# Kernel tuning notes

Measured on AMD Instinct MI355X. Metric: run time of the kernel, lower is better.

## Reference

```python
import jax, jax.numpy as jnp
import numpy as np

N = 100000   # nodes
E = 1600000  # edges (avg degree 16)
D = 128      # feature dim (layer_sizes = [128, 128, 128])


def setup_inputs() -> dict:
    key = jax.random.key(0)
    ks = jax.random.split(key, 8)
    s = 1.0 / np.sqrt(D)  # glorot-ish scale for linear weights
    return {
        "x": jax.random.normal(ks[0], (N, D), jnp.float32),
        "edge_index": jax.random.randint(ks[1], (2, E), 0, N, dtype=jnp.int32),
        "perturb_first": jax.random.normal(ks[2], (N, D), jnp.float32) * 0.01,
        "perturb_last": jax.random.normal(ks[3], (N, D), jnp.float32) * 0.01,
        "W1": jax.random.normal(ks[4], (D, D), jnp.float32) * s,
        "b1": jnp.zeros((D,), jnp.float32),
        "W2": jax.random.normal(ks[5], (D, D), jnp.float32) * s,
        "b2": jnp.zeros((D,), jnp.float32),
    }


def reference(x, edge_index, perturb_first, perturb_last, W1, b1, W2, b2):
    n = x.shape[0]
    # PyG GCNConv: add self-loops, symmetric deg^{-1/2} normalization.
    loop = jnp.arange(n, dtype=edge_index.dtype)
    src = jnp.concatenate([edge_index[0], loop])  # [E+N]
    dst = jnp.concatenate([edge_index[1], loop])  # [E+N]
    deg = jax.ops.segment_sum(jnp.ones(dst.shape[0], x.dtype), dst, num_segments=n)
    dinv = jnp.where(deg > 0, 1.0 / jnp.sqrt(deg), 0.0)
    norm = (dinv[src] * dinv[dst])[:, None]  # [E+N, 1]

    def gcn_conv(h, W, b):
        h = h @ W.T                                   # linear (bias-free), [N, D]
        msg = h[src] * norm                           # gather + scale, [E+N, D]
        out = jax.ops.segment_sum(msg, dst, num_segments=n)  # scatter-add
        return out + b

    # forward only runs model[0] and model[3] (the two GCNConv layers);
    # norms and PReLU are skipped by the original forward.
    h = gcn_conv(x, W1, b1) + perturb_first
    out = gcn_conv(h, W2, b2) + perturb_last
    return out
```

## Files before the change

kernel.cpp:

```cpp
#include <hip/hip_runtime.h>
#include <math.h>

#define D 128
#define WS_PAD 132

typedef short bf16x8 __attribute__((ext_vector_type(8)));
typedef float f32x4 __attribute__((ext_vector_type(4)));

__device__ __forceinline__ unsigned short f2bf(float f) {
  unsigned u = __float_as_uint(f);
  u += 0x7FFFu + ((u >> 16) & 1u);
  return (unsigned short)(u >> 16);
}

__device__ __forceinline__ float bf2f(unsigned short h) {
  return __uint_as_float(((unsigned)h) << 16);
}

__device__ __forceinline__ float bflo(unsigned u) { return __uint_as_float(u << 16); }
__device__ __forceinline__ float bfhi(unsigned u) { return __uint_as_float(u & 0xFFFF0000u); }


__global__ __launch_bounds__(256) void count_deg_kernel(const int* __restrict__ dst, int E,
                                                        int* __restrict__ deg,
                                                        int* __restrict__ rank,
                                                        const float* __restrict__ W2,
                                                        unsigned short* __restrict__ W2bf,
                                                        const float* __restrict__ W1,
                                                        unsigned short* __restrict__ W1h,
                                                        unsigned short* __restrict__ W1l) {
  int nbe = (E + 1023) >> 10;
  int b = blockIdx.x;
  if (b >= nbe) {
    if (W2bf == nullptr) return;
    int which = b - nbe;
    if (which < 8) {
      int t = which * 256 + threadIdx.x;
      #pragma unroll
      for (int q = 0; q < 2; ++q) {
        int idx = t + q * 2048;
        float4 w = ((const float4*)W2)[idx];
        ushort4 o;
        o.x = f2bf(w.x); o.y = f2bf(w.y); o.z = f2bf(w.z); o.w = f2bf(w.w);
        ((ushort4*)W2bf)[idx] = o;
      }
    } else {
      int t = (which - 8) * 256 + threadIdx.x;
      #pragma unroll
      for (int q = 0; q < 2; ++q) {
        int idx = t + q * 2048;
        float4 w = ((const float4*)W1)[idx];
        ushort4 hi, lo;
        hi.x = f2bf(w.x); lo.x = f2bf(w.x - bf2f(hi.x));
        hi.y = f2bf(w.y); lo.y = f2bf(w.y - bf2f(hi.y));
        hi.z = f2bf(w.z); lo.z = f2bf(w.z - bf2f(hi.z));
        hi.w = f2bf(w.w); lo.w = f2bf(w.w - bf2f(hi.w));
        ((ushort4*)W1h)[idx] = hi;
        ((ushort4*)W1l)[idx] = lo;
      }
    }
    return;
  }
  int e0 = (b * 256 + threadIdx.x) * 4;
  if (rank != nullptr) {
    if (e0 + 4 <= E && ((E & 3) == 0)) {
      int4 d = *(const int4*)(dst + e0);
      int r0 = atomicAdd(&deg[d.x], 1);
      int r1 = atomicAdd(&deg[d.y], 1);
      int r2 = atomicAdd(&deg[d.z], 1);
      int r3 = atomicAdd(&deg[d.w], 1);
      *(int4*)(rank + e0) = make_int4(r0, r1, r2, r3);
    } else {
      for (int e = e0; e < E && e < e0 + 4; ++e) rank[e] = atomicAdd(&deg[dst[e]], 1);
    }
  } else {
    for (int e = e0; e < E && e < e0 + 4; ++e) atomicAdd(&deg[dst[e]], 1);
  }
}


__global__ __launch_bounds__(256) void scan_blocksum_kernel(const int* __restrict__ deg, int n,
                                                            int* __restrict__ blockSums) {
  __shared__ int sm[256];
  int t = threadIdx.x;
  int i = blockIdx.x * 256 + t;
  sm[t] = (i < n) ? deg[i] : 0;
  __syncthreads();
  for (int off = 128; off > 0; off >>= 1) {
    if (t < off) sm[t] += sm[t + off];
    __syncthreads();
  }
  if (t == 0) blockSums[blockIdx.x] = sm[0];
}

__global__ __launch_bounds__(512) void scan_top_kernel(int* __restrict__ blockSums, int nb) {
  __shared__ int sm[512];
  int t = threadIdx.x;
  int v = (t < nb) ? blockSums[t] : 0;
  sm[t] = v;
  __syncthreads();
  for (int off = 1; off < 512; off <<= 1) {
    int x = (t >= off) ? sm[t - off] : 0;
    __syncthreads();
    sm[t] += x;
    __syncthreads();
  }
  if (t < nb) blockSums[t] = sm[t] - v;
}

__global__ __launch_bounds__(256) void scan_write_kernel(const int* __restrict__ deg, int n,
                                                         const int* __restrict__ blockSums,
                                                         int* __restrict__ ptr,
                                                         float* __restrict__ dinv) {
  __shared__ int sm[256];
  int t = threadIdx.x;
  int i = blockIdx.x * 256 + t;
  int v = (i < n) ? deg[i] : 0;
  sm[t] = v;
  __syncthreads();
  for (int off = 1; off < 256; off <<= 1) {
    int x = (t >= off) ? sm[t - off] : 0;
    __syncthreads();
    sm[t] += x;
    __syncthreads();
  }
  if (i < n) {
    int ex = blockSums[blockIdx.x] + sm[t] - v;
    ptr[i] = ex;
    dinv[i] = 1.0f / sqrtf((float)(v + 1));
    if (i == n - 1) ptr[n] = ex + v;
  }
}


__device__ __forceinline__ void gemm_body(const float* __restrict__ X,
                                          const float* __restrict__ W,
                                          const float* __restrict__ dinv,
                                          unsigned short* __restrict__ H, int n,
                                          int bid, int nblocks,
                                          float* __restrict__ Ws, float* __restrict__ Xs) {
  const int tid = threadIdx.x;
  const int tx = tid & 31;
  const int ty = tid >> 5;
  const int ntiles = (n + 31) >> 5;

  for (int tile = bid; tile < ntiles; tile += nblocks) {
    const int row0 = tile << 5;
    const int rows_here = min(32, n - row0);
    __syncthreads();
    {
      const float4* Xg = (const float4*)(X + (size_t)row0 * D);
      int tmax = rows_here * 32;
      for (int t = tid; t < tmax; t += 256) ((float4*)Xs)[t] = Xg[t];
    }
    float acc[4][4] = {{0.f}};
    #pragma unroll
    for (int kt = 0; kt < 128; kt += 64) {
      __syncthreads();
      for (int t = tid; t < 2048; t += 256) {
        int j  = t >> 4;
        int k4 = (t & 15) << 2;
        float4 w = ((const float4*)W)[j * 32 + (kt >> 2) + (t & 15)];
        Ws[(k4 + 0) * WS_PAD + j] = w.x;
        Ws[(k4 + 1) * WS_PAD + j] = w.y;
        Ws[(k4 + 2) * WS_PAD + j] = w.z;
        Ws[(k4 + 3) * WS_PAD + j] = w.w;
      }
      __syncthreads();
      #pragma unroll 4
      for (int k = 0; k < 64; ++k) {
        float4 w = *(const float4*)&Ws[k * WS_PAD + (tx << 2)];
        #pragma unroll
        for (int r = 0; r < 4; ++r) {
          float xv = Xs[(ty + 8 * r) * 128 + (kt + k)];
          acc[r][0] += xv * w.x;
          acc[r][1] += xv * w.y;
          acc[r][2] += xv * w.z;
          acc[r][3] += xv * w.w;
        }
      }
    }
    #pragma unroll
    for (int r = 0; r < 4; ++r) {
      int row = row0 + ty + 8 * r;
      if (row < n) {
        float s = dinv[row];
        unsigned h0 = f2bf(s * acc[r][0]);
        unsigned h1 = f2bf(s * acc[r][1]);
        unsigned h2 = f2bf(s * acc[r][2]);
        unsigned h3 = f2bf(s * acc[r][3]);
        ((uint2*)(H + (size_t)row * D))[tx] = make_uint2(h0 | (h1 << 16), h2 | (h3 << 16));
      }
    }
  }
}


__global__ __launch_bounds__(256) void fused_fill_gemm_kernel(
    const int* __restrict__ src, const int* __restrict__ dst,
    int* __restrict__ ptr, int* __restrict__ csr, int E,
    const float* __restrict__ X, const float* __restrict__ W,
    const float* __restrict__ dinv, unsigned short* __restrict__ H, int n) {
  __shared__ float Ws[64 * WS_PAD];
  __shared__ float Xs[32 * 128];
  int sub = blockIdx.x & 7;
  if (sub < 2) {
    int fb = (blockIdx.x >> 3) * 2 + sub;
    int stride = 512 * 256;
    for (int e = fb * 256 + threadIdx.x; e < E; e += stride) {
      int d = dst[e];
      int pos = atomicAdd(&ptr[d], 1);
      csr[pos] = src[e];
    }
  } else {
    int gb = (blockIdx.x >> 3) * 6 + (sub - 2);
    gemm_body(X, W, dinv, H, n, gb, 1536, Ws, Xs);
  }
}

__global__ __launch_bounds__(256) void gemm128_kernel(const float* __restrict__ X,
                                                      const float* __restrict__ W,
                                                      const float* __restrict__ dinv,
                                                      unsigned short* __restrict__ H, int n) {
  __shared__ float Ws[64 * WS_PAD];
  __shared__ float Xs[32 * 128];
  gemm_body(X, W, dinv, H, n, blockIdx.x, gridDim.x, Ws, Xs);
}


#define FUSED_GRID 2048
#define G1_PITCH 136

__global__ __launch_bounds__(256) void fused_fill_mfma_kernel(
    const int* __restrict__ src, const int* __restrict__ dst,
    const int* __restrict__ ptr, const int* __restrict__ rank,
    int* __restrict__ csr, int E,
    const float* __restrict__ X,
    const unsigned short* __restrict__ W1h, const unsigned short* __restrict__ W1l,
    const float* __restrict__ dinv, unsigned short* __restrict__ H, int n) {
  __shared__ unsigned short Ths[32 * G1_PITCH];
  __shared__ unsigned short Tls[32 * G1_PITCH];
  int sub = blockIdx.x & 7;
  if (sub < 2) {
    int fb = (blockIdx.x >> 3) * 2 + sub;
    const int T8 = 512 * 256 * 8;
    int t = fb * 256 + threadIdx.x;
    const bool al16 = ((E & 3) == 0);
    for (int e0 = t * 8; e0 < E; e0 += T8) {
      if (e0 + 8 <= E && al16) {
        int4 d0 = ((const int4*)(dst + e0))[0];
        int4 d1 = ((const int4*)(dst + e0))[1];
        int4 s0 = ((const int4*)(src + e0))[0];
        int4 s1 = ((const int4*)(src + e0))[1];
        int4 r0 = ((const int4*)(rank + e0))[0];
        int4 r1 = ((const int4*)(rank + e0))[1];
        int p0 = ptr[d0.x] + r0.x;
        int p1 = ptr[d0.y] + r0.y;
        int p2 = ptr[d0.z] + r0.z;
        int p3 = ptr[d0.w] + r0.w;
        int p4 = ptr[d1.x] + r1.x;
        int p5 = ptr[d1.y] + r1.y;
        int p6 = ptr[d1.z] + r1.z;
        int p7 = ptr[d1.w] + r1.w;
        csr[p0] = s0.x; csr[p1] = s0.y; csr[p2] = s0.z; csr[p3] = s0.w;
        csr[p4] = s1.x; csr[p5] = s1.y; csr[p6] = s1.z; csr[p7] = s1.w;
      } else {
        for (int e = e0; e < E && e < e0 + 8; ++e)
          csr[ptr[dst[e]] + rank[e]] = src[e];
      }
    }
  } else {
    int gb = (blockIdx.x >> 3) * 6 + (sub - 2);
    const int tid = threadIdx.x;
    const int wv = tid >> 6;
    const int lane = tid & 63;
    const int m = lane & 15;
    const int quad = lane >> 4;
    const int mt = wv >> 1;
    const int ntb = (wv & 1) * 4;
    const int ntiles = (n + 31) >> 5;

    for (int tile = gb; tile < ntiles; tile += 1536) {
      const int row0 = tile << 5;
      const int rows_here = min(32, n - row0);
      __syncthreads();
      {
        const float4* Xg = (const float4*)(X + (size_t)row0 * D);
        int tmax = rows_here * 32;
        for (int t = tid; t < tmax; t += 256) {
          float4 xv = Xg[t];
          int r = t >> 5, c4 = (t & 31) << 2;
          ushort4 hi, lo;
          hi.x = f2bf(xv.x); lo.x = f2bf(xv.x - bf2f(hi.x));
          hi.y = f2bf(xv.y); lo.y = f2bf(xv.y - bf2f(hi.y));
          hi.z = f2bf(xv.z); lo.z = f2bf(xv.z - bf2f(hi.z));
          hi.w = f2bf(xv.w); lo.w = f2bf(xv.w - bf2f(hi.w));
          *(ushort4*)&Ths[r * G1_PITCH + c4] = hi;
          *(ushort4*)&Tls[r * G1_PITCH + c4] = lo;
        }
      }
      __syncthreads();

      f32x4 acc0 = {0.f, 0.f, 0.f, 0.f};
      f32x4 acc1 = {0.f, 0.f, 0.f, 0.f};
      f32x4 acc2 = {0.f, 0.f, 0.f, 0.f};
      f32x4 acc3 = {0.f, 0.f, 0.f, 0.f};
      #pragma unroll
      for (int s = 0; s < 4; ++s) {
        int k = (s << 5) + (quad << 3);
        bf16x8 ah = *(const bf16x8*)&Ths[(mt * 16 + m) * G1_PITCH + k];
        bf16x8 al = *(const bf16x8*)&Tls[(mt * 16 + m) * G1_PITCH + k];
        bf16x8 bh0 = *(const bf16x8*)&W1h[(size_t)((ntb + 0) * 16 + m) * 128 + k];
        bf16x8 bl0 = *(const bf16x8*)&W1l[(size_t)((ntb + 0) * 16 + m) * 128 + k];
        acc0 = __builtin_amdgcn_mfma_f32_16x16x32_bf16(ah, bh0, acc0, 0, 0, 0);
        acc0 = __builtin_amdgcn_mfma_f32_16x16x32_bf16(al, bh0, acc0, 0, 0, 0);
        acc0 = __builtin_amdgcn_mfma_f32_16x16x32_bf16(ah, bl0, acc0, 0, 0, 0);
        bf16x8 bh1 = *(const bf16x8*)&W1h[(size_t)((ntb + 1) * 16 + m) * 128 + k];
        bf16x8 bl1 = *(const bf16x8*)&W1l[(size_t)((ntb + 1) * 16 + m) * 128 + k];
        acc1 = __builtin_amdgcn_mfma_f32_16x16x32_bf16(ah, bh1, acc1, 0, 0, 0);
        acc1 = __builtin_amdgcn_mfma_f32_16x16x32_bf16(al, bh1, acc1, 0, 0, 0);
        acc1 = __builtin_amdgcn_mfma_f32_16x16x32_bf16(ah, bl1, acc1, 0, 0, 0);
        bf16x8 bh2 = *(const bf16x8*)&W1h[(size_t)((ntb + 2) * 16 + m) * 128 + k];
        bf16x8 bl2 = *(const bf16x8*)&W1l[(size_t)((ntb + 2) * 16 + m) * 128 + k];
        acc2 = __builtin_amdgcn_mfma_f32_16x16x32_bf16(ah, bh2, acc2, 0, 0, 0);
        acc2 = __builtin_amdgcn_mfma_f32_16x16x32_bf16(al, bh2, acc2, 0, 0, 0);
        acc2 = __builtin_amdgcn_mfma_f32_16x16x32_bf16(ah, bl2, acc2, 0, 0, 0);
        bf16x8 bh3 = *(const bf16x8*)&W1h[(size_t)((ntb + 3) * 16 + m) * 128 + k];
        bf16x8 bl3 = *(const bf16x8*)&W1l[(size_t)((ntb + 3) * 16 + m) * 128 + k];
        acc3 = __builtin_amdgcn_mfma_f32_16x16x32_bf16(ah, bh3, acc3, 0, 0, 0);
        acc3 = __builtin_amdgcn_mfma_f32_16x16x32_bf16(al, bh3, acc3, 0, 0, 0);
        acc3 = __builtin_amdgcn_mfma_f32_16x16x32_bf16(ah, bl3, acc3, 0, 0, 0);
      }
      #pragma unroll
      for (int r = 0; r < 4; ++r) {
        int row = mt * 16 + (quad << 2) + r;
        int g = row0 + row;
        if (g < n) {
          float sc = dinv[g];
          H[(size_t)g * D + (ntb + 0) * 16 + m] = f2bf(sc * acc0[r]);
          H[(size_t)g * D + (ntb + 1) * 16 + m] = f2bf(sc * acc1[r]);
          H[(size_t)g * D + (ntb + 2) * 16 + m] = f2bf(sc * acc2[r]);
          H[(size_t)g * D + (ntb + 3) * 16 + m] = f2bf(sc * acc3[r]);
        }
      }
    }
  }
}


__device__ __forceinline__ void gather_quad(const int* __restrict__ csr, int start, int end,
                                            const uint4* __restrict__ Hu4, int i, int sub,
                                            float acc[8]) {
  uint4 v = Hu4[(size_t)i * 16 + sub];
  acc[0] = bflo(v.x); acc[1] = bfhi(v.x);
  acc[2] = bflo(v.y); acc[3] = bfhi(v.y);
  acc[4] = bflo(v.z); acc[5] = bfhi(v.z);
  acc[6] = bflo(v.w); acc[7] = bfhi(v.w);
  int e = start;
  while (__ballot(e < end)) {
    uint4 w0 = {0u, 0u, 0u, 0u}, w1 = {0u, 0u, 0u, 0u};
    if (e < end)     w0 = Hu4[(size_t)csr[e] * 16 + sub];
    if (e + 1 < end) w1 = Hu4[(size_t)csr[e + 1] * 16 + sub];
    acc[0] += bflo(w0.x); acc[1] += bfhi(w0.x);
    acc[2] += bflo(w0.y); acc[3] += bfhi(w0.y);
    acc[4] += bflo(w0.z); acc[5] += bfhi(w0.z);
    acc[6] += bflo(w0.w); acc[7] += bfhi(w0.w);
    acc[0] += bflo(w1.x); acc[1] += bfhi(w1.x);
    acc[2] += bflo(w1.y); acc[3] += bfhi(w1.y);
    acc[4] += bflo(w1.z); acc[5] += bfhi(w1.z);
    acc[6] += bflo(w1.w); acc[7] += bfhi(w1.w);
    e += 2;
  }
}


__device__ __forceinline__ void gather_row_legacy(const int* __restrict__ csr, int start, int end,
                                                  const unsigned* __restrict__ Hu,
                                                  int i, int lane, float& ax, float& ay) {
  unsigned v = Hu[(size_t)i * 64 + lane];
  ax = __uint_as_float(v << 16);
  ay = __uint_as_float(v & 0xFFFF0000u);
  for (int e = start; e < end; ++e) {
    unsigned w = Hu[(size_t)csr[e] * 64 + lane];
    ax += __uint_as_float(w << 16);
    ay += __uint_as_float(w & 0xFFFF0000u);
  }
}


__global__ __launch_bounds__(256, 8) void gather_kernel(const int* __restrict__ csr,
                                                        const int* __restrict__ rptr,
                                                        const float* __restrict__ dinv,
                                                        const unsigned* __restrict__ Hu,
                                                        const float* __restrict__ bias,
                                                        const float* __restrict__ perturb,
                                                        float* __restrict__ out, int n) {
  const int lane = threadIdx.x & 63;
  const int g = lane >> 4;
  const int sub = lane & 15;
  int i = (blockIdx.x << 4) + ((threadIdx.x >> 6) << 2) + g;
  bool valid = i < n;
  int ic = valid ? i : (n - 1);
  int start = rptr[ic];
  int end = valid ? rptr[ic + 1] : start;
  float acc[8];
  gather_quad(csr, start, end, (const uint4*)Hu, ic, sub, acc);
  if (valid) {
    float di = dinv[i];
    float4 b0 = *(const float4*)&bias[sub * 8];
    float4 b1 = *(const float4*)&bias[sub * 8 + 4];
    float4 p0 = *(const float4*)&perturb[(size_t)i * D + sub * 8];
    float4 p1 = *(const float4*)&perturb[(size_t)i * D + sub * 8 + 4];
    float4 o0, o1;
    o0.x = b0.x + p0.x + di * acc[0];
    o0.y = b0.y + p0.y + di * acc[1];
    o0.z = b0.z + p0.z + di * acc[2];
    o0.w = b0.w + p0.w + di * acc[3];
    o1.x = b1.x + p1.x + di * acc[4];
    o1.y = b1.y + p1.y + di * acc[5];
    o1.z = b1.z + p1.z + di * acc[6];
    o1.w = b1.w + p1.w + di * acc[7];
    *(float4*)&out[(size_t)i * D + sub * 8] = o0;
    *(float4*)&out[(size_t)i * D + sub * 8 + 4] = o1;
  }
}

__global__ __launch_bounds__(256, 8) void gather_kernel_old(const int* __restrict__ csr,
                                                            const int* __restrict__ rend,
                                                            const float* __restrict__ dinv,
                                                            const unsigned* __restrict__ Hu,
                                                            const float* __restrict__ bias,
                                                            const float* __restrict__ perturb,
                                                            float* __restrict__ out, int n) {
  int i = (blockIdx.x << 2) + (threadIdx.x >> 6);
  if (i >= n) return;
  int lane = threadIdx.x & 63;
  int start = (i == 0) ? 0 : rend[i - 1];
  float ax, ay;
  gather_row_legacy(csr, start, rend[i], Hu, i, lane, ax, ay);
  float di = dinv[i];
  float2 p = ((const float2*)(perturb + (size_t)i * D))[lane];
  float2 o;
  o.x = bias[2 * lane + 0] + p.x + di * ax;
  o.y = bias[2 * lane + 1] + p.y + di * ay;
  ((float2*)(out + (size_t)i * D))[lane] = o;
}


#define GG_PITCH 136

__global__ __launch_bounds__(512, 8) void gather_gemm_kernel(
    const int* __restrict__ csr, const int* __restrict__ rptr,
    const float* __restrict__ dinv, const unsigned* __restrict__ Hu,
    const float* __restrict__ bias, const float* __restrict__ perturb,
    const unsigned short* __restrict__ W2bf, unsigned short* __restrict__ H2, int n) {
  __shared__ unsigned short Ts[32 * GG_PITCH];
  const int tid = threadIdx.x;
  const int wv = tid >> 6;
  const int lane = tid & 63;
  const int base = blockIdx.x << 5;

  {
    const int g = lane >> 4;
    const int sub = lane & 15;
    int row_in_block = (wv << 2) + g;
    int i = base + row_in_block;
    bool valid = i < n;
    int ic = valid ? i : (n - 1);
    int start = rptr[ic];
    int end = valid ? rptr[ic + 1] : start;
    float acc[8];
    gather_quad(csr, start, end, (const uint4*)Hu, ic, sub, acc);
    if (valid) {
      float di = dinv[i];
      float4 b0 = *(const float4*)&bias[sub * 8];
      float4 b1 = *(const float4*)&bias[sub * 8 + 4];
      float4 p0 = *(const float4*)&perturb[(size_t)i * D + sub * 8];
      float4 p1 = *(const float4*)&perturb[(size_t)i * D + sub * 8 + 4];
      unsigned q0 = (unsigned)f2bf(b0.x + p0.x + di * acc[0]) |
                    ((unsigned)f2bf(b0.y + p0.y + di * acc[1]) << 16);
      unsigned q1 = (unsigned)f2bf(b0.z + p0.z + di * acc[2]) |
                    ((unsigned)f2bf(b0.w + p0.w + di * acc[3]) << 16);
      unsigned q2 = (unsigned)f2bf(b1.x + p1.x + di * acc[4]) |
                    ((unsigned)f2bf(b1.y + p1.y + di * acc[5]) << 16);
      unsigned q3 = (unsigned)f2bf(b1.z + p1.z + di * acc[6]) |
                    ((unsigned)f2bf(b1.w + p1.w + di * acc[7]) << 16);
      uint4 pack = make_uint4(q0, q1, q2, q3);
      *(uint4*)&Ts[row_in_block * GG_PITCH + sub * 8] = pack;
    }
  }
  __syncthreads();

  const int mt = wv >> 2;
  const int nt0 = wv & 3;
  const int m = lane & 15;
  const int quad = lane >> 4;
  const unsigned short* Wrow0 = W2bf + (size_t)(nt0 * 16 + m) * 128;
  const unsigned short* Wrow1 = W2bf + (size_t)((nt0 + 4) * 16 + m) * 128;
  f32x4 acc0 = {0.f, 0.f, 0.f, 0.f};
  f32x4 acc1 = {0.f, 0.f, 0.f, 0.f};
  #pragma unroll
  for (int s = 0; s < 4; ++s) {
    int k = (s << 5) + (quad << 3);
    bf16x8 a  = *(const bf16x8*)&Ts[(mt * 16 + m) * GG_PITCH + k];
    bf16x8 b0 = *(const bf16x8*)&Wrow0[k];
    bf16x8 b1 = *(const bf16x8*)&Wrow1[k];
    acc0 = __builtin_amdgcn_mfma_f32_16x16x32_bf16(a, b0, acc0, 0, 0, 0);
    acc1 = __builtin_amdgcn_mfma_f32_16x16x32_bf16(a, b1, acc1, 0, 0, 0);
  }
  #pragma unroll
  for (int r = 0; r < 4; ++r) {
    int row = mt * 16 + (quad << 2) + r;
    int gg = base + row;
    if (gg < n) {
      float s = dinv[gg];
      H2[(size_t)gg * D + nt0 * 16 + m]       = f2bf(s * acc0[r]);
      H2[(size_t)gg * D + (nt0 + 4) * 16 + m] = f2bf(s * acc1[r]);
    }
  }
}


extern "C" void kernel_launch(void* const* d_in, const int* in_sizes, int n_in,
                              void* d_out, int out_size, void* d_ws, size_t ws_size,
                              hipStream_t stream) {
  const float* x  = (const float*)d_in[0];
  const int*   ei = (const int*)d_in[1];
  const float* pf = (const float*)d_in[2];
  const float* pl = (const float*)d_in[3];
  const float* W1 = (const float*)d_in[4];
  const float* b1 = (const float*)d_in[5];
  const float* W2 = (const float*)d_in[6];
  const float* b2 = (const float*)d_in[7];
  float* out = (float*)d_out;

  const int n = in_sizes[0] / D;
  const int E = in_sizes[1] / 2;
  const int* src = ei;
  const int* dst = ei + E;

  int*   deg       = (int*)d_ws;
  float* dinv      = (float*)d_ws + n;
  int*   ptr       = (int*)d_ws + 2 * n;
  int*   blockSums = (int*)d_ws + 3 * n + 1;
  int*   csr       = (int*)d_ws + 3 * n + 1 + 512;
  size_t a1_off = ((size_t)(3 * n + 1 + 512 + E) * 4 + 255) & ~(size_t)255;
  unsigned short* A1 = (unsigned short*)((char*)d_ws + a1_off);
  unsigned short* A2 = A1 + (size_t)n * D;
  unsigned short* W2bf = A2 + (size_t)n * D;
  unsigned short* W1h  = W2bf + 128 * 128;
  unsigned short* W1l  = W1h + 128 * 128;
  int* rank = (int*)A2;
  size_t needed = a1_off + (2 * (size_t)n * D + 3 * 128 * 128) * sizeof(unsigned short);
  const bool fused_l2 = (ws_size >= needed);

  const int nb_n = (n + 255) / 256;
  const int nb_e4 = (E + 1023) / 1024;
  const int nb_g16 = (n + 15) / 16;
  const int nb_g4 = (n + 3) / 4;

  hipMemsetAsync(deg, 0, (size_t)n * sizeof(int), stream);
  count_deg_kernel<<<nb_e4 + 16, 256, 0, stream>>>(
      dst, E, deg, fused_l2 ? rank : (int*)nullptr, W2,
      fused_l2 ? W2bf : (unsigned short*)nullptr, W1, W1h, W1l);
  scan_blocksum_kernel<<<nb_n, 256, 0, stream>>>(deg, n, blockSums);
  scan_top_kernel<<<1, 512, 0, stream>>>(blockSums, nb_n);
  scan_write_kernel<<<nb_n, 256, 0, stream>>>(deg, n, blockSums, ptr, dinv);

  if (fused_l2) {
    fused_fill_mfma_kernel<<<FUSED_GRID, 256, 0, stream>>>(src, dst, ptr, rank, csr, E, x,
                                                           W1h, W1l, dinv, A1, n);
    gather_gemm_kernel<<<(n + 31) / 32, 512, 0, stream>>>(csr, ptr, dinv, (const unsigned*)A1,
                                                          b1, pf, W2bf, A2, n);
    gather_kernel<<<nb_g16, 256, 0, stream>>>(csr, ptr, dinv, (const unsigned*)A2, b2, pl, out, n);
  } else {
    fused_fill_gemm_kernel<<<FUSED_GRID, 256, 0, stream>>>(src, dst, ptr, csr, E, x, W1, dinv, A1, n);
    gather_kernel_old<<<nb_g4, 256, 0, stream>>>(csr, ptr, dinv, (const unsigned*)A1, b1, pf, out, n);
    gemm128_kernel<<<1024, 256, 0, stream>>>(out, W2, dinv, A1, n);
    gather_kernel_old<<<nb_g4, 256, 0, stream>>>(csr, ptr, dinv, (const unsigned*)A1, b2, pl, out, n);
  }
}
```

Measured before the change: 490.5 us.

## Overlap degree counting with layer-1 GEMM and apply source normalization in gather

The layer-1 MFMA GEMM now writes unscaled X·W1 and runs fused with the degree-count atomics, so it no longer waits for the degree scan and dinv. The per-source dinv scaling moves into the first gather, which now loads dinv[j] for every neighbor, and CSR fill becomes its own kernel after the scan. Weight conversion is split out into a small separate kernel. The trade is an extra random dinv load per edge in gather 1 and one more launch, in exchange for overlapping the atomic-heavy count with the GEMM.

New measurement: 460.2 us. -6.2%, faster.

```diff
diff --git a/kernel.cpp b/kernel.cpp
--- a/kernel.cpp
+++ b/kernel.cpp
@@ -21,256 +21,70 @@
 __device__ __forceinline__ float bfhi(unsigned u) { return __uint_as_float(u & 0xFFFF0000u); }
 
 
-__global__ __launch_bounds__(256) void count_deg_kernel(const int* __restrict__ dst, int E,
-                                                        int* __restrict__ deg,
-                                                        int* __restrict__ rank,
-                                                        const float* __restrict__ W2,
-                                                        unsigned short* __restrict__ W2bf,
-                                                        const float* __restrict__ W1,
-                                                        unsigned short* __restrict__ W1h,
-                                                        unsigned short* __restrict__ W1l) {
-  int nbe = (E + 1023) >> 10;
-  int b = blockIdx.x;
-  if (b >= nbe) {
-    if (W2bf == nullptr) return;
-    int which = b - nbe;
-    if (which < 8) {
-      int t = which * 256 + threadIdx.x;
-      #pragma unroll
-      for (int q = 0; q < 2; ++q) {
-        int idx = t + q * 2048;
-        float4 w = ((const float4*)W2)[idx];
-        ushort4 o;
-        o.x = f2bf(w.x); o.y = f2bf(w.y); o.z = f2bf(w.z); o.w = f2bf(w.w);
-        ((ushort4*)W2bf)[idx] = o;
-      }
-    } else {
-      int t = (which - 8) * 256 + threadIdx.x;
-      #pragma unroll
-      for (int q = 0; q < 2; ++q) {
-        int idx = t + q * 2048;
-        float4 w = ((const float4*)W1)[idx];
-        ushort4 hi, lo;
-        hi.x = f2bf(w.x); lo.x = f2bf(w.x - bf2f(hi.x));
-        hi.y = f2bf(w.y); lo.y = f2bf(w.y - bf2f(hi.y));
-        hi.z = f2bf(w.z); lo.z = f2bf(w.z - bf2f(hi.z));
-        hi.w = f2bf(w.w); lo.w = f2bf(w.w - bf2f(hi.w));
-        ((ushort4*)W1h)[idx] = hi;
-        ((ushort4*)W1l)[idx] = lo;
-      }
-    }
-    return;
-  }
-  int e0 = (b * 256 + threadIdx.x) * 4;
-  if (rank != nullptr) {
-    if (e0 + 4 <= E && ((E & 3) == 0)) {
-      int4 d = *(const int4*)(dst + e0);
-      int r0 = atomicAdd(&deg[d.x], 1);
-      int r1 = atomicAdd(&deg[d.y], 1);
-      int r2 = atomicAdd(&deg[d.z], 1);
-      int r3 = atomicAdd(&deg[d.w], 1);
-      *(int4*)(rank + e0) = make_int4(r0, r1, r2, r3);
-    } else {
-      for (int e = e0; e < E && e < e0 + 4; ++e) rank[e] = atomicAdd(&deg[dst[e]], 1);
+__global__ __launch_bounds__(256) void wprep_kernel(const float* __restrict__ W2,
+                                                    unsigned short* __restrict__ W2bf,
+                                                    const float* __restrict__ W1,
+                                                    unsigned short* __restrict__ W1h,
+                                                    unsigned short* __restrict__ W1l) {
+  int which = blockIdx.x;
+  if (which < 8) {
+    int t = which * 256 + threadIdx.x;
+    #pragma unroll
+    for (int q = 0; q < 2; ++q) {
+      int idx = t + q * 2048;
+      float4 w = ((const float4*)W2)[idx];
+      ushort4 o;
+      o.x = f2bf(w.x); o.y = f2bf(w.y); o.z = f2bf(w.z); o.w = f2bf(w.w);
+      ((ushort4*)W2bf)[idx] = o;
     }
   } else {
-    for (int e = e0; e < E && e < e0 + 4; ++e) atomicAdd(&deg[dst[e]], 1);
-  }
-}
-
-
-__global__ __launch_bounds__(256) void scan_blocksum_kernel(const int* __restrict__ deg, int n,
-                                                            int* __restrict__ blockSums) {
-  __shared__ int sm[256];
-  int t = threadIdx.x;
-  int i = blockIdx.x * 256 + t;
-  sm[t] = (i < n) ? deg[i] : 0;
-  __syncthreads();
-  for (int off = 128; off > 0; off >>= 1) {
-    if (t < off) sm[t] += sm[t + off];
-    __syncthreads();
-  }
-  if (t == 0) blockSums[blockIdx.x] = sm[0];
-}
-
-__global__ __launch_bounds__(512) void scan_top_kernel(int* __restrict__ blockSums, int nb) {
-  __shared__ int sm[512];
-  int t = threadIdx.x;
-  int v = (t < nb) ? blockSums[t] : 0;
-  sm[t] = v;
-  __syncthreads();
-  for (int off = 1; off < 512; off <<= 1) {
-    int x = (t >= off) ? sm[t - off] : 0;
-    __syncthreads();
-    sm[t] += x;
-    __syncthreads();
-  }
-  if (t < nb) blockSums[t] = sm[t] - v;
-}
-
-__global__ __launch_bounds__(256) void scan_write_kernel(const int* __restrict__ deg, int n,
-                                                         const int* __restrict__ blockSums,
-                                                         int* __restrict__ ptr,
-                                                         float* __restrict__ dinv) {
-  __shared__ int sm[256];
-  int t = threadIdx.x;
-  int i = blockIdx.x * 256 + t;
-  int v = (i < n) ? deg[i] : 0;
-  sm[t] = v;
-  __syncthreads();
-  for (int off = 1; off < 256; off <<= 1) {
-    int x = (t >= off) ? sm[t - off] : 0;
-    __syncthreads();
-    sm[t] += x;
-    __syncthreads();
-  }
-  if (i < n) {
-    int ex = blockSums[blockIdx.x] + sm[t] - v;
-    ptr[i] = ex;
-    dinv[i] = 1.0f / sqrtf((float)(v + 1));
-    if (i == n - 1) ptr[n] = ex + v;
-  }
-}
-
-
-__device__ __forceinline__ void gemm_body(const float* __restrict__ X,
-                                          const float* __restrict__ W,
-                                          const float* __restrict__ dinv,
-                                          unsigned short* __restrict__ H, int n,
-                                          int bid, int nblocks,
-                                          float* __restrict__ Ws, float* __restrict__ Xs) {
-  const int tid = threadIdx.x;
-  const int tx = tid & 31;
-  const int ty = tid >> 5;
-  const int ntiles = (n + 31) >> 5;
-
-  for (int tile = bid; tile < ntiles; tile += nblocks) {
-    const int row0 = tile << 5;
-    const int rows_here = min(32, n - row0);
-    __syncthreads();
-    {
-      const float4* Xg = (const float4*)(X + (size_t)row0 * D);
-      int tmax = rows_here * 32;
-      for (int t = tid; t < tmax; t += 256) ((float4*)Xs)[t] = Xg[t];
-    }
-    float acc[4][4] = {{0.f}};
+    int t = (which - 8) * 256 + threadIdx.x;
     #pragma unroll
-    for (int kt = 0; kt < 128; kt += 64) {
-      __syncthreads();
-      for (int t = tid; t < 2048; t += 256) {
-        int j  = t >> 4;
-        int k4 = (t & 15) << 2;
-        float4 w = ((const float4*)W)[j * 32 + (kt >> 2) + (t & 15)];
-        Ws[(k4 + 0) * WS_PAD + j] = w.x;
-        Ws[(k4 + 1) * WS_PAD + j] = w.y;
-        Ws[(k4 + 2) * WS_PAD + j] = w.z;
-        Ws[(k4 + 3) * WS_PAD + j] = w.w;
-      }
-      __syncthreads();
-      #pragma unroll 4
-      for (int k = 0; k < 64; ++k) {
-        float4 w = *(const float4*)&Ws[k * WS_PAD + (tx << 2)];
-        #pragma unroll
-        for (int r = 0; r < 4; ++r) {
-          float xv = Xs[(ty + 8 * r) * 128 + (kt + k)];
-          acc[r][0] += xv * w.x;
-          acc[r][1] += xv * w.y;
-          acc[r][2] += xv * w.z;
-          acc[r][3] += xv * w.w;
-        }
-      }
-    }
-    #pragma unroll
-    for (int r = 0; r < 4; ++r) {
-      int row = row0 + ty + 8 * r;
-      if (row < n) {
-        float s = dinv[row];
-        unsigned h0 = f2bf(s * acc[r][0]);
-        unsigned h1 = f2bf(s * acc[r][1]);
-        unsigned h2 = f2bf(s * acc[r][2]);
-        unsigned h3 = f2bf(s * acc[r][3]);
-        ((uint2*)(H + (size_t)row * D))[tx] = make_uint2(h0 | (h1 << 16), h2 | (h3 << 16));
-      }
-    }
-  }
-}
-
-
-__global__ __launch_bounds__(256) void fused_fill_gemm_kernel(
-    const int* __restrict__ src, const int* __restrict__ dst,
-    int* __restrict__ ptr, int* __restrict__ csr, int E,
-    const float* __restrict__ X, const float* __restrict__ W,
-    const float* __restrict__ dinv, unsigned short* __restrict__ H, int n) {
-  __shared__ float Ws[64 * WS_PAD];
-  __shared__ float Xs[32 * 128];
-  int sub = blockIdx.x & 7;
-  if (sub < 2) {
-    int fb = (blockIdx.x >> 3) * 2 + sub;
-    int stride = 512 * 256;
-    for (int e = fb * 256 + threadIdx.x; e < E; e += stride) {
-      int d = dst[e];
-      int pos = atomicAdd(&ptr[d], 1);
-      csr[pos] = src[e];
-    }
-  } else {
-    int gb = (blockIdx.x >> 3) * 6 + (sub - 2);
-    gemm_body(X, W, dinv, H, n, gb, 1536, Ws, Xs);
-  }
-}
-
-__global__ __launch_bounds__(256) void gemm128_kernel(const float* __restrict__ X,
-                                                      const float* __restrict__ W,
-                                                      const float* __restrict__ dinv,
-                                                      unsigned short* __restrict__ H, int n) {
-  __shared__ float Ws[64 * WS_PAD];
-  __shared__ float Xs[32 * 128];
-  gemm_body(X, W, dinv, H, n, blockIdx.x, gridDim.x, Ws, Xs);
+    for (int q = 0; q < 2; ++q) {
+      int idx = t + q * 2048;
+      float4 w = ((const float4*)W1)[idx];
+      ushort4 hi, lo;
+      hi.x = f2bf(w.x); lo.x = f2bf(w.x - bf2f(hi.x));
+      hi.y = f2bf(w.y); lo.y = f2bf(w.y - bf2f(hi.y));
+      hi.z = f2bf(w.z); lo.z = f2bf(w.z - bf2f(hi.z));
+      hi.w = f2bf(w.w); lo.w = f2bf(w.w - bf2f(hi.w));
+      ((ushort4*)W1h)[idx] = hi;
+      ((ushort4*)W1l)[idx] = lo;
+    }
+  }
 }
 
 
 #define FUSED_GRID 2048
 #define G1_PITCH 136
 
-__global__ __launch_bounds__(256) void fused_fill_mfma_kernel(
-    const int* __restrict__ src, const int* __restrict__ dst,
-    const int* __restrict__ ptr, const int* __restrict__ rank,
-    int* __restrict__ csr, int E,
+__global__ __launch_bounds__(256) void count_gemm1_kernel(
+    const int* __restrict__ dst, int E, int* __restrict__ deg, int* __restrict__ rank,
     const float* __restrict__ X,
     const unsigned short* __restrict__ W1h, const unsigned short* __restrict__ W1l,
-    const float* __restrict__ dinv, unsigned short* __restrict__ H, int n) {
+    unsigned short* __restrict__ H, int n) {
   __shared__ unsigned short Ths[32 * G1_PITCH];
   __shared__ unsigned short Tls[32 * G1_PITCH];
   int sub = blockIdx.x & 7;
-  if (sub < 2) {
-    int fb = (blockIdx.x >> 3) * 2 + sub;
-    const int T8 = 512 * 256 * 8;
-    int t = fb * 256 + threadIdx.x;
+  if (sub < 4) {
+    int cb = (blockIdx.x >> 3) * 4 + sub;
+    const int T4 = 1024 * 256 * 4;
+    int t = cb * 256 + threadIdx.x;
     const bool al16 = ((E & 3) == 0);
-    for (int e0 = t * 8; e0 < E; e0 += T8) {
-      if (e0 + 8 <= E && al16) {
-        int4 d0 = ((const int4*)(dst + e0))[0];
-        int4 d1 = ((const int4*)(dst + e0))[1];
-        int4 s0 = ((const int4*)(src + e0))[0];
-        int4 s1 = ((const int4*)(src + e0))[1];
-        int4 r0 = ((const int4*)(rank + e0))[0];
-        int4 r1 = ((const int4*)(rank + e0))[1];
-        int p0 = ptr[d0.x] + r0.x;
-        int p1 = ptr[d0.y] + r0.y;
-        int p2 = ptr[d0.z] + r0.z;
-        int p3 = ptr[d0.w] + r0.w;
-        int p4 = ptr[d1.x] + r1.x;
-        int p5 = ptr[d1.y] + r1.y;
-        int p6 = ptr[d1.z] + r1.z;
-        int p7 = ptr[d1.w] + r1.w;
-        csr[p0] = s0.x; csr[p1] = s0.y; csr[p2] = s0.z; csr[p3] = s0.w;
-        csr[p4] = s1.x; csr[p5] = s1.y; csr[p6] = s1.z; csr[p7] = s1.w;
+    for (int e0 = t * 4; e0 < E; e0 += T4) {
+      if (e0 + 4 <= E && al16) {
+        int4 d = *(const int4*)(dst + e0);
+        int r0 = atomicAdd(&deg[d.x], 1);
+        int r1 = atomicAdd(&deg[d.y], 1);
+        int r2 = atomicAdd(&deg[d.z], 1);
+        int r3 = atomicAdd(&deg[d.w], 1);
+        *(int4*)(rank + e0) = make_int4(r0, r1, r2, r3);
       } else {
-        for (int e = e0; e < E && e < e0 + 8; ++e)
-          csr[ptr[dst[e]] + rank[e]] = src[e];
+        for (int e = e0; e < E && e < e0 + 4; ++e) rank[e] = atomicAdd(&deg[dst[e]], 1);
       }
     }
   } else {
-    int gb = (blockIdx.x >> 3) * 6 + (sub - 2);
+    int gb = (blockIdx.x >> 3) * 4 + (sub - 4);
     const int tid = threadIdx.x;
     const int wv = tid >> 6;
     const int lane = tid & 63;
@@ -280,7 +94,7 @@
     const int ntb = (wv & 1) * 4;
     const int ntiles = (n + 31) >> 5;
 
-    for (int tile = gb; tile < ntiles; tile += 1536) {
+    for (int tile = gb; tile < ntiles; tile += 1024) {
       const int row0 = tile << 5;
       const int rows_here = min(32, n - row0);
       __syncthreads();
@@ -336,15 +150,235 @@
         int row = mt * 16 + (quad << 2) + r;
         int g = row0 + row;
         if (g < n) {
-          float sc = dinv[g];
-          H[(size_t)g * D + (ntb + 0) * 16 + m] = f2bf(sc * acc0[r]);
-          H[(size_t)g * D + (ntb + 1) * 16 + m] = f2bf(sc * acc1[r]);
-          H[(size_t)g * D + (ntb + 2) * 16 + m] = f2bf(sc * acc2[r]);
-          H[(size_t)g * D + (ntb + 3) * 16 + m] = f2bf(sc * acc3[r]);
+          H[(size_t)g * D + (ntb + 0) * 16 + m] = f2bf(acc0[r]);
+          H[(size_t)g * D + (ntb + 1) * 16 + m] = f2bf(acc1[r]);
+          H[(size_t)g * D + (ntb + 2) * 16 + m] = f2bf(acc2[r]);
+          H[(size_t)g * D + (ntb + 3) * 16 + m] = f2bf(acc3[r]);
         }
       }
     }
   }
+}
+
+
+__global__ __launch_bounds__(256) void fill_kernel(const int* __restrict__ src,
+                                                   const int* __restrict__ dst,
+                                                   const int* __restrict__ ptr,
+                                                   const int* __restrict__ rank,
+                                                   int* __restrict__ csr, int E) {
+  const int T8 = FUSED_GRID * 256 * 8;
+  int t = blockIdx.x * 256 + threadIdx.x;
+  const bool al16 = ((E & 3) == 0);
+  for (int e0 = t * 8; e0 < E; e0 += T8) {
+    if (e0 + 8 <= E && al16) {
+      int4 d0 = ((const int4*)(dst + e0))[0];
+      int4 d1 = ((const int4*)(dst + e0))[1];
+      int4 s0 = ((const int4*)(src + e0))[0];
+      int4 s1 = ((const int4*)(src + e0))[1];
+      int4 r0 = ((const int4*)(rank + e0))[0];
+      int4 r1 = ((const int4*)(rank + e0))[1];
+      csr[ptr[d0.x] + r0.x] = s0.x;
+      csr[ptr[d0.y] + r0.y] = s0.y;
+      csr[ptr[d0.z] + r0.z] = s0.z;
+      csr[ptr[d0.w] + r0.w] = s0.w;
+      csr[ptr[d1.x] + r1.x] = s1.x;
+      csr[ptr[d1.y] + r1.y] = s1.y;
+      csr[ptr[d1.z] + r1.z] = s1.z;
+      csr[ptr[d1.w] + r1.w] = s1.w;
+    } else {
+      for (int e = e0; e < E && e < e0 + 8; ++e)
+        csr[ptr[dst[e]] + rank[e]] = src[e];
+    }
+  }
+}
+
+
+__global__ __launch_bounds__(256) void scan_blocksum_kernel(const int* __restrict__ deg, int n,
+                                                            int* __restrict__ blockSums) {
+  __shared__ int sm[256];
+  int t = threadIdx.x;
+  int i = blockIdx.x * 256 + t;
+  sm[t] = (i < n) ? deg[i] : 0;
+  __syncthreads();
+  for (int off = 128; off > 0; off >>= 1) {
+    if (t < off) sm[t] += sm[t + off];
+    __syncthreads();
+  }
+  if (t == 0) blockSums[blockIdx.x] = sm[0];
+}
+
+__global__ __launch_bounds__(512) void scan_top_kernel(int* __restrict__ blockSums, int nb) {
+  __shared__ int sm[512];
+  int t = threadIdx.x;
+  int v = (t < nb) ? blockSums[t] : 0;
+  sm[t] = v;
+  __syncthreads();
+  for (int off = 1; off < 512; off <<= 1) {
+    int x = (t >= off) ? sm[t - off] : 0;
+    __syncthreads();
+    sm[t] += x;
+    __syncthreads();
+  }
+  if (t < nb) blockSums[t] = sm[t] - v;
+}
+
+__global__ __launch_bounds__(256) void scan_write_kernel(const int* __restrict__ deg, int n,
+                                                         const int* __restrict__ blockSums,
+                                                         int* __restrict__ ptr,
+                                                         float* __restrict__ dinv) {
+  __shared__ int sm[256];
+  int t = threadIdx.x;
+  int i = blockIdx.x * 256 + t;
+  int v = (i < n) ? deg[i] : 0;
+  sm[t] = v;
+  __syncthreads();
+  for (int off = 1; off < 256; off <<= 1) {
+    int x = (t >= off) ? sm[t - off] : 0;
+    __syncthreads();
+    sm[t] += x;
+    __syncthreads();
+  }
+  if (i < n) {
+    int ex = blockSums[blockIdx.x] + sm[t] - v;
+    ptr[i] = ex;
+    dinv[i] = 1.0f / sqrtf((float)(v + 1));
+    if (i == n - 1) ptr[n] = ex + v;
+  }
+}
+
+
+__device__ __forceinline__ void gemm_body(const float* __restrict__ X,
+                                          const float* __restrict__ W,
+                                          const float* __restrict__ dinv,
+                                          unsigned short* __restrict__ H, int n,
+                                          int bid, int nblocks,
+                                          float* __restrict__ Ws, float* __restrict__ Xs) {
+  const int tid = threadIdx.x;
+  const int tx = tid & 31;
+  const int ty = tid >> 5;
+  const int ntiles = (n + 31) >> 5;
+
+  for (int tile = bid; tile < ntiles; tile += nblocks) {
+    const int row0 = tile << 5;
+    const int rows_here = min(32, n - row0);
+    __syncthreads();
+    {
+      const float4* Xg = (const float4*)(X + (size_t)row0 * D);
+      int tmax = rows_here * 32;
+      for (int t = tid; t < tmax; t += 256) ((float4*)Xs)[t] = Xg[t];
+    }
+    float acc[4][4] = {{0.f}};
+    #pragma unroll
+    for (int kt = 0; kt < 128; kt += 64) {
+      __syncthreads();
+      for (int t = tid; t < 2048; t += 256) {
+        int j  = t >> 4;
+        int k4 = (t & 15) << 2;
+        float4 w = ((const float4*)W)[j * 32 + (kt >> 2) + (t & 15)];
+        Ws[(k4 + 0) * WS_PAD + j] = w.x;
+        Ws[(k4 + 1) * WS_PAD + j] = w.y;
+        Ws[(k4 + 2) * WS_PAD + j] = w.z;
+        Ws[(k4 + 3) * WS_PAD + j] = w.w;
+      }
+      __syncthreads();
+      #pragma unroll 4
+      for (int k = 0; k < 64; ++k) {
+        float4 w = *(const float4*)&Ws[k * WS_PAD + (tx << 2)];
+        #pragma unroll
+        for (int r = 0; r < 4; ++r) {
+          float xv = Xs[(ty + 8 * r) * 128 + (kt + k)];
+          acc[r][0] += xv * w.x;
+          acc[r][1] += xv * w.y;
+          acc[r][2] += xv * w.z;
+          acc[r][3] += xv * w.w;
+        }
+      }
+    }
+    #pragma unroll
+    for (int r = 0; r < 4; ++r) {
+      int row = row0 + ty + 8 * r;
+      if (row < n) {
+        float s = dinv[row];
+        unsigned h0 = f2bf(s * acc[r][0]);
+        unsigned h1 = f2bf(s * acc[r][1]);
+        unsigned h2 = f2bf(s * acc[r][2]);
+        unsigned h3 = f2bf(s * acc[r][3]);
+        ((uint2*)(H + (size_t)row * D))[tx] = make_uint2(h0 | (h1 << 16), h2 | (h3 << 16));
+      }
+    }
+  }
+}
+
+
+__global__ __launch_bounds__(256) void count_legacy_kernel(const int* __restrict__ dst, int E,
+                                                           int* __restrict__ deg) {
+  int e = blockIdx.x * 256 + threadIdx.x;
+  if (e < E) atomicAdd(&deg[dst[e]], 1);
+}
+
+__global__ __launch_bounds__(256) void fused_fill_gemm_kernel(
+    const int* __restrict__ src, const int* __restrict__ dst,
+    int* __restrict__ ptr, int* __restrict__ csr, int E,
+    const float* __restrict__ X, const float* __restrict__ W,
+    const float* __restrict__ dinv, unsigned short* __restrict__ H, int n) {
+  __shared__ float Ws[64 * WS_PAD];
+  __shared__ float Xs[32 * 128];
+  int sub = blockIdx.x & 7;
+  if (sub < 2) {
+    int fb = (blockIdx.x >> 3) * 2 + sub;
+    int stride = 512 * 256;
+    for (int e = fb * 256 + threadIdx.x; e < E; e += stride) {
+      int d = dst[e];
+      int pos = atomicAdd(&ptr[d], 1);
+      csr[pos] = src[e];
+    }
+  } else {
+    int gb = (blockIdx.x >> 3) * 6 + (sub - 2);
+    gemm_body(X, W, dinv, H, n, gb, 1536, Ws, Xs);
+  }
+}
+
+__global__ __launch_bounds__(256) void gemm128_kernel(const float* __restrict__ X,
+                                                      const float* __restrict__ W,
+                                                      const float* __restrict__ dinv,
+                                                      unsigned short* __restrict__ H, int n) {
+  __shared__ float Ws[64 * WS_PAD];
+  __shared__ float Xs[32 * 128];
+  gemm_body(X, W, dinv, H, n, blockIdx.x, gridDim.x, Ws, Xs);
+}
+
+__device__ __forceinline__ void gather_row_legacy(const int* __restrict__ csr, int start, int end,
+                                                  const unsigned* __restrict__ Hu,
+                                                  int i, int lane, float& ax, float& ay) {
+  unsigned v = Hu[(size_t)i * 64 + lane];
+  ax = __uint_as_float(v << 16);
+  ay = __uint_as_float(v & 0xFFFF0000u);
+  for (int e = start; e < end; ++e) {
+    unsigned w = Hu[(size_t)csr[e] * 64 + lane];
+    ax += __uint_as_float(w << 16);
+    ay += __uint_as_float(w & 0xFFFF0000u);
+  }
+}
+
+__global__ __launch_bounds__(256, 8) void gather_kernel_old(const int* __restrict__ csr,
+                                                            const int* __restrict__ rend,
+                                                            const float* __restrict__ dinv,
+                                                            const unsigned* __restrict__ Hu,
+                                                            const float* __restrict__ bias,
+                                                            const float* __restrict__ perturb,
+                                                            float* __restrict__ out, int n) {
+  int i = (blockIdx.x << 2) + (threadIdx.x >> 6);
+  if (i >= n) return;
+  int lane = threadIdx.x & 63;
+  int start = (i == 0) ? 0 : rend[i - 1];
+  float ax, ay;
+  gather_row_legacy(csr, start, rend[i], Hu, i, lane, ax, ay);
+  float di = dinv[i];
+  float2 p = ((const float2*)(perturb + (size_t)i * D))[lane];
+  float2 o;
+  o.x = bias[2 * lane + 0] + p.x + di * ax;
+  o.y = bias[2 * lane + 1] + p.y + di * ay;
+  ((float2*)(out + (size_t)i * D))[lane] = o;
 }
 
 
@@ -373,17 +407,31 @@
   }
 }
 
-
-__device__ __forceinline__ void gather_row_legacy(const int* __restrict__ csr, int start, int end,
-                                                  const unsigned* __restrict__ Hu,
-                                                  int i, int lane, float& ax, float& ay) {
-  unsigned v = Hu[(size_t)i * 64 + lane];
-  ax = __uint_as_float(v << 16);
-  ay = __uint_as_float(v & 0xFFFF0000u);
-  for (int e = start; e < end; ++e) {
-    unsigned w = Hu[(size_t)csr[e] * 64 + lane];
-    ax += __uint_as_float(w << 16);
-    ay += __uint_as_float(w & 0xFFFF0000u);
+__device__ __forceinline__ void gather_quad_w(const int* __restrict__ csr, int start, int end,
+                                              const uint4* __restrict__ Hu4,
+                                              const float* __restrict__ dinv,
+                                              int i, int sub, float acc[8]) {
+  float ds = dinv[i];
+  uint4 v = Hu4[(size_t)i * 16 + sub];
+  acc[0] = ds * bflo(v.x); acc[1] = ds * bfhi(v.x);
+  acc[2] = ds * bflo(v.y); acc[3] = ds * bfhi(v.y);
+  acc[4] = ds * bflo(v.z); acc[5] = ds * bfhi(v.z);
+  acc[6] = ds * bflo(v.w); acc[7] = ds * bfhi(v.w);
+  int e = start;
+  while (__ballot(e < end)) {
+    uint4 w0 = {0u, 0u, 0u, 0u}, w1 = {0u, 0u, 0u, 0u};
+    float d0 = 0.f, d1 = 0.f;
+    if (e < end)     { int j = csr[e];     w0 = Hu4[(size_t)j * 16 + sub]; d0 = dinv[j]; }
+    if (e + 1 < end) { int j = csr[e + 1]; w1 = Hu4[(size_t)j * 16 + sub]; d1 = dinv[j]; }
+    acc[0] += d0 * bflo(w0.x); acc[1] += d0 * bfhi(w0.x);
+    acc[2] += d0 * bflo(w0.y); acc[3] += d0 * bfhi(w0.y);
+    acc[4] += d0 * bflo(w0.z); acc[5] += d0 * bfhi(w0.z);
+    acc[6] += d0 * bflo(w0.w); acc[7] += d0 * bfhi(w0.w);
+    acc[0] += d1 * bflo(w1.x); acc[1] += d1 * bfhi(w1.x);
+    acc[2] += d1 * bflo(w1.y); acc[3] += d1 * bfhi(w1.y);
+    acc[4] += d1 * bflo(w1.z); acc[5] += d1 * bfhi(w1.z);
+    acc[6] += d1 * bflo(w1.w); acc[7] += d1 * bfhi(w1.w);
+    e += 2;
   }
 }
 
@@ -425,27 +473,6 @@
   }
 }
 
-__global__ __launch_bounds__(256, 8) void gather_kernel_old(const int* __restrict__ csr,
-                                                            const int* __restrict__ rend,
-                                                            const float* __restrict__ dinv,
-                                                            const unsigned* __restrict__ Hu,
-                                                            const float* __restrict__ bias,
-                                                            const float* __restrict__ perturb,
-                                                            float* __restrict__ out, int n) {
-  int i = (blockIdx.x << 2) + (threadIdx.x >> 6);
-  if (i >= n) return;
-  int lane = threadIdx.x & 63;
-  int start = (i == 0) ? 0 : rend[i - 1];
-  float ax, ay;
-  gather_row_legacy(csr, start, rend[i], Hu, i, lane, ax, ay);
-  float di = dinv[i];
-  float2 p = ((const float2*)(perturb + (size_t)i * D))[lane];
-  float2 o;
-  o.x = bias[2 * lane + 0] + p.x + di * ax;
-  o.y = bias[2 * lane + 1] + p.y + di * ay;
-  ((float2*)(out + (size_t)i * D))[lane] = o;
-}
-
 
 #define GG_PITCH 136
 
@@ -470,7 +497,7 @@
     int start = rptr[ic];
     int end = valid ? rptr[ic + 1] : start;
     float acc[8];
-    gather_quad(csr, start, end, (const uint4*)Hu, ic, sub, acc);
+    gather_quad_w(csr, start, end, (const uint4*)Hu, dinv, ic, sub, acc);
     if (valid) {
       float di = dinv[i];
       float4 b0 = *(const float4*)&bias[sub * 8];
@@ -555,25 +582,27 @@
   const bool fused_l2 = (ws_size >= needed);
 
   const int nb_n = (n + 255) / 256;
-  const int nb_e4 = (E + 1023) / 1024;
+  const int nb_e = (E + 255) / 256;
   const int nb_g16 = (n + 15) / 16;
   const int nb_g4 = (n + 3) / 4;
 
   hipMemsetAsync(deg, 0, (size_t)n * sizeof(int), stream);
-  count_deg_kernel<<<nb_e4 + 16, 256, 0, stream>>>(
-      dst, E, deg, fused_l2 ? rank : (int*)nullptr, W2,
-      fused_l2 ? W2bf : (unsigned short*)nullptr, W1, W1h, W1l);
-  scan_blocksum_kernel<<<nb_n, 256, 0, stream>>>(deg, n, blockSums);
-  scan_top_kernel<<<1, 512, 0, stream>>>(blockSums, nb_n);
-  scan_write_kernel<<<nb_n, 256, 0, stream>>>(deg, n, blockSums, ptr, dinv);
 
   if (fused_l2) {
-    fused_fill_mfma_kernel<<<FUSED_GRID, 256, 0, stream>>>(src, dst, ptr, rank, csr, E, x,
-                                                           W1h, W1l, dinv, A1, n);
+    wprep_kernel<<<16, 256, 0, stream>>>(W2, W2bf, W1, W1h, W1l);
+    count_gemm1_kernel<<<FUSED_GRID, 256, 0, stream>>>(dst, E, deg, rank, x, W1h, W1l, A1, n);
+    scan_blocksum_kernel<<<nb_n, 256, 0, stream>>>(deg, n, blockSums);
+    scan_top_kernel<<<1, 512, 0, stream>>>(blockSums, nb_n);
+    scan_write_kernel<<<nb_n, 256, 0, stream>>>(deg, n, blockSums, ptr, dinv);
+    fill_kernel<<<FUSED_GRID, 256, 0, stream>>>(src, dst, ptr, rank, csr, E);
     gather_gemm_kernel<<<(n + 31) / 32, 512, 0, stream>>>(csr, ptr, dinv, (const unsigned*)A1,
                                                           b1, pf, W2bf, A2, n);
     gather_kernel<<<nb_g16, 256, 0, stream>>>(csr, ptr, dinv, (const unsigned*)A2, b2, pl, out, n);
   } else {
+    count_legacy_kernel<<<nb_e, 256, 0, stream>>>(dst, E, deg);
+    scan_blocksum_kernel<<<nb_n, 256, 0, stream>>>(deg, n, blockSums);
+    scan_top_kernel<<<1, 512, 0, stream>>>(blockSums, nb_n);
+    scan_write_kernel<<<nb_n, 256, 0, stream>>>(deg, n, blockSums, ptr, dinv);
     fused_fill_gemm_kernel<<<FUSED_GRID, 256, 0, stream>>>(src, dst, ptr, csr, E, x, W1, dinv, A1, n);
     gather_kernel_old<<<nb_g4, 256, 0, stream>>>(csr, ptr, dinv, (const unsigned*)A1, b1, pf, out, n);
     gemm128_kernel<<<1024, 256, 0, stream>>>(out, W2, dinv, A1, n);
```
